# Optimization experiments

Measured on AMD Instinct MI355X. Metric: run time of the kernel, lower is better.

The kernel has to match this reference:

```python
import jax, jax.numpy as jnp
import numpy as np


def _mlp(x, W1, b1, W2, b2, W3, b3):
    # flatten -> fc(784,512) -> relu -> fc(512,128) -> relu -> fc(128,C)
    h = x.reshape(x.shape[0], -1)
    h = jax.nn.relu(h @ W1.T + b1)
    h = jax.nn.relu(h @ W2.T + b2)
    return h @ W3.T + b3


def setup_inputs() -> dict:
    key = jax.random.key(0)
    ks = jax.random.split(key, 6)
    B, Bu, C, D = 65536, 4096, 10, 28 * 28
    return {
        "x": jax.random.uniform(ks[0], (B, 28, 28), jnp.float32),
        "y": jax.random.randint(ks[1], (B,), 0, C),
        "x_unlab": jax.random.uniform(ks[2], (Bu, 28, 28), jnp.float32),
        "W1": jax.random.normal(ks[3], (512, D), jnp.float32) * 0.03,
        "b1": jnp.zeros((512,), jnp.float32),
        "W2": jax.random.normal(ks[4], (128, 512), jnp.float32) * 0.05,
        "b2": jnp.zeros((128,), jnp.float32),
        "W3": jax.random.normal(ks[5], (C, 128), jnp.float32) * 0.08,
        "b3": jnp.zeros((C,), jnp.float32),
    }


def reference(x, y, x_unlab, W1, b1, W2, b2, W3, b3):
    n_classes = W3.shape[0]
    # ---- labeled branch: BCEWithLogitsLoss(mean) vs one-hot targets ----
    logits = _mlp(x, W1, b1, W2, b2, W3, b3)  # [B, C]
    t = jax.nn.one_hot(y, n_classes, dtype=logits.dtype)
    bce = jnp.mean(jnp.maximum(logits, 0.0) - logits * t
                   + jnp.log1p(jnp.exp(-jnp.abs(logits))))
    # ---- unlabeled branch: semantic loss ----
    # sem_loss(probs): s[c] = sum_i p_i[c] * prod_{j != i} (1 - p_j[c]);
    # return mean over classes of -log(s). Done in log domain with a single
    # O(Bu) leave-one-out sum instead of the original O(Bu^2) double loop.
    o_u = _mlp(x_unlab, W1, b1, W2, b2, W3, b3)       # [Bu, C]
    logp = jax.nn.log_sigmoid(o_u)                     # log p
    log1mp = jax.nn.log_sigmoid(-o_u)                  # log (1 - p)
    loo = jnp.sum(log1mp, axis=0, keepdims=True) - log1mp  # leave-one-out log-prod
    log_s = jax.scipy.special.logsumexp(logp + loo, axis=0)  # [C]
    sl = jnp.mean(-log_s)
    # compute_loss returns (bce, sl); stacked here as a length-2 vector
    return jnp.stack([bce, sl])
```

## Files before the change

kernel.cpp:

```cpp
#include <hip/hip_runtime.h>
#include <hip/hip_bf16.h>
#include <stdint.h>

typedef unsigned short ushort_t;
typedef __bf16 bf16x8 __attribute__((ext_vector_type(8)));
typedef float f32x4 __attribute__((ext_vector_type(4)));

__device__ __forceinline__ ushort_t f2bf(float f) {
    union { float f; unsigned u; } v; v.f = f;
    unsigned u = v.u;
    unsigned r = u + 0x7fffu + ((u >> 16) & 1u);
    return (ushort_t)(r >> 16);
}
__device__ __forceinline__ float bf2f(ushort_t h) {
    union { unsigned u; float f; } v; v.u = ((unsigned)h) << 16;
    return v.f;
}

#define GLDS16(gsrc, ldst)                                                    \
    __builtin_amdgcn_global_load_lds(                                         \
        (const __attribute__((address_space(1))) void*)(gsrc),                \
        (__attribute__((address_space(3))) void*)(ldst), 16, 0, 0)

__global__ __launch_bounds__(256) void prep_kernel(
    const float* __restrict__ W1, const float* __restrict__ W2,
    ushort_t* __restrict__ W1p, ushort_t* __restrict__ W2b,
    float* __restrict__ stats)
{
    int idx = blockIdx.x * 256 + threadIdx.x;
    if (idx < 512 * 800) {
        int n = idx / 800, k = idx - n * 800;
        W1p[idx] = (k < 784) ? f2bf(W1[n * 784 + k]) : (ushort_t)0;
    }
    if (idx < 128 * 512) W2b[idx] = f2bf(W2[idx]);
    if (idx == 0) stats[0] = 0.0f;
}

__global__ __launch_bounds__(256) void gemm1_kernel(
    const float* __restrict__ x, const float* __restrict__ xu,
    const ushort_t* __restrict__ W1p, const float* __restrict__ b1,
    ushort_t* __restrict__ h1)
{
    __shared__ ushort_t As[128 * 32];
    __shared__ ushort_t Bs[128 * 32];

    const int tile_n = blockIdx.x & 3;
    const int tile_m = blockIdx.x >> 2;
    const int tid = threadIdx.x;
    const int w = tid >> 6, lane = tid & 63;
    const int wm = w >> 1, wn = w & 1;
    const int quad = lane >> 4, lc = lane & 15;

    const int arow = tid >> 1;
    const int akoff = (tid & 1) * 16;
    const int grow = tile_m * 128 + arow;
    const float* asrc = (grow < 65536) ? (x + (size_t)grow * 784)
                                       : (xu + (size_t)(grow - 65536) * 784);
    const int brow_in = (lane >> 2);
    const int bkoff = (lane & 3) * 8;

    f32x4 acc[4][4];
#pragma unroll
    for (int i = 0; i < 4; i++)
#pragma unroll
        for (int j = 0; j < 4; j++)
#pragma unroll
            for (int r = 0; r < 4; r++) acc[i][j][r] = 0.0f;

    for (int k0 = 0; k0 < 800; k0 += 32) {
#pragma unroll
        for (int c = 0; c < 2; c++) {
            int row = (w * 2 + c) * 16 + brow_in;
            const ushort_t* src =
                W1p + (size_t)(tile_n * 128 + row) * 800 + k0 + bkoff;
            GLDS16(src, Bs + (w * 2 + c) * 512);
        }
        {
            int kch = k0 + akoff;
            uint4 lo, hi;
            if (kch < 784) {
                const float4* p = (const float4*)(asrc + kch);
                float4 f0 = p[0], f1 = p[1], f2 = p[2], f3 = p[3];
                lo.x = ((unsigned)f2bf(f0.y) << 16) | f2bf(f0.x);
                lo.y = ((unsigned)f2bf(f0.w) << 16) | f2bf(f0.z);
                lo.z = ((unsigned)f2bf(f1.y) << 16) | f2bf(f1.x);
                lo.w = ((unsigned)f2bf(f1.w) << 16) | f2bf(f1.z);
                hi.x = ((unsigned)f2bf(f2.y) << 16) | f2bf(f2.x);
                hi.y = ((unsigned)f2bf(f2.w) << 16) | f2bf(f2.z);
                hi.z = ((unsigned)f2bf(f3.y) << 16) | f2bf(f3.x);
                hi.w = ((unsigned)f2bf(f3.w) << 16) | f2bf(f3.z);
            } else {
                lo = make_uint4(0, 0, 0, 0);
                hi = make_uint4(0, 0, 0, 0);
            }
            *(uint4*)&As[arow * 32 + akoff] = lo;
            *(uint4*)&As[arow * 32 + akoff + 8] = hi;
        }
        __syncthreads();

        bf16x8 af[4], bfr[4];
#pragma unroll
        for (int i = 0; i < 4; i++)
            af[i] = *(const bf16x8*)&As[(wm * 64 + i * 16 + lc) * 32 + quad * 8];
#pragma unroll
        for (int j = 0; j < 4; j++)
            bfr[j] = *(const bf16x8*)&Bs[(wn * 64 + j * 16 + lc) * 32 + quad * 8];
#pragma unroll
        for (int i = 0; i < 4; i++)
#pragma unroll
            for (int j = 0; j < 4; j++)
                acc[i][j] = __builtin_amdgcn_mfma_f32_16x16x32_bf16(
                    af[i], bfr[j], acc[i][j], 0, 0, 0);
        __syncthreads();
    }

    float bias[4];
#pragma unroll
    for (int j = 0; j < 4; j++)
        bias[j] = b1[tile_n * 128 + wn * 64 + j * 16 + lc];
#pragma unroll
    for (int i = 0; i < 4; i++) {
        int gr0 = tile_m * 128 + wm * 64 + i * 16 + quad * 4;
#pragma unroll
        for (int j = 0; j < 4; j++) {
            int gc = tile_n * 128 + wn * 64 + j * 16 + lc;
#pragma unroll
            for (int r = 0; r < 4; r++) {
                float v = acc[i][j][r] + bias[j];
                v = fmaxf(v, 0.0f);
                h1[(size_t)(gr0 + r) * 512 + gc] = f2bf(v);
            }
        }
    }
}

__global__ __launch_bounds__(256) void gemm2_kernel(
    const ushort_t* __restrict__ h1, const ushort_t* __restrict__ W2b,
    const float* __restrict__ b2, ushort_t* __restrict__ h2)
{
    __shared__ ushort_t As[128 * 32];
    __shared__ ushort_t Bs[128 * 32];

    const int tile_m = blockIdx.x;
    const int tid = threadIdx.x;
    const int w = tid >> 6, lane = tid & 63;
    const int wm = w >> 1, wn = w & 1;
    const int quad = lane >> 4, lc = lane & 15;
    const int row_in = (lane >> 2);
    const int koff = (lane & 3) * 8;

    f32x4 acc[4][4];
#pragma unroll
    for (int i = 0; i < 4; i++)
#pragma unroll
        for (int j = 0; j < 4; j++)
#pragma unroll
            for (int r = 0; r < 4; r++) acc[i][j][r] = 0.0f;

    for (int k0 = 0; k0 < 512; k0 += 32) {
#pragma unroll
        for (int c = 0; c < 2; c++) {
            int row = (w * 2 + c) * 16 + row_in;
            const ushort_t* srcA =
                h1 + (size_t)(tile_m * 128 + row) * 512 + k0 + koff;
            GLDS16(srcA, As + (w * 2 + c) * 512);
            const ushort_t* srcB = W2b + (size_t)row * 512 + k0 + koff;
            GLDS16(srcB, Bs + (w * 2 + c) * 512);
        }
        __syncthreads();

        bf16x8 af[4], bfr[4];
#pragma unroll
        for (int i = 0; i < 4; i++)
            af[i] = *(const bf16x8*)&As[(wm * 64 + i * 16 + lc) * 32 + quad * 8];
#pragma unroll
        for (int j = 0; j < 4; j++)
            bfr[j] = *(const bf16x8*)&Bs[(wn * 64 + j * 16 + lc) * 32 + quad * 8];
#pragma unroll
        for (int i = 0; i < 4; i++)
#pragma unroll
            for (int j = 0; j < 4; j++)
                acc[i][j] = __builtin_amdgcn_mfma_f32_16x16x32_bf16(
                    af[i], bfr[j], acc[i][j], 0, 0, 0);
        __syncthreads();
    }

    float bias[4];
#pragma unroll
    for (int j = 0; j < 4; j++) bias[j] = b2[wn * 64 + j * 16 + lc];
#pragma unroll
    for (int i = 0; i < 4; i++) {
        int gr0 = tile_m * 128 + wm * 64 + i * 16 + quad * 4;
#pragma unroll
        for (int j = 0; j < 4; j++) {
            int gc = wn * 64 + j * 16 + lc;
#pragma unroll
            for (int r = 0; r < 4; r++) {
                float v = acc[i][j][r] + bias[j];
                v = fmaxf(v, 0.0f);
                h2[(size_t)(gr0 + r) * 128 + gc] = f2bf(v);
            }
        }
    }
}

__global__ __launch_bounds__(256) void loss_kernel(
    const ushort_t* __restrict__ h2, const int* __restrict__ y,
    const float* __restrict__ W3, const float* __restrict__ b3,
    float* __restrict__ stats, float* __restrict__ logits_u)
{
    __shared__ float W3s[10 * 128];
    __shared__ float b3s[10];
    __shared__ ushort_t h2s[64 * 128];
    __shared__ float red[4];

    const int tid = threadIdx.x;
    for (int i = tid; i < 1280; i += 256) W3s[i] = W3[i];
    if (tid < 10) b3s[tid] = b3[tid];

    const size_t row0 = (size_t)blockIdx.x * 64;
    const ushort_t* src = h2 + row0 * 128;
#pragma unroll
    for (int i = tid * 8; i < 64 * 128; i += 256 * 8)
        *(uint4*)&h2s[i] = *(const uint4*)&src[i];
    __syncthreads();

    float bce_part = 0.0f;
    for (int o = tid; o < 640; o += 256) {
        int r = o / 10, c = o - r * 10;
        size_t grow = row0 + r;
        float acc = b3s[c];
        const ushort_t* hr = &h2s[r * 128];
        const float* wr = &W3s[c * 128];
#pragma unroll 8
        for (int k = 0; k < 128; k++) acc += bf2f(hr[k]) * wr[k];
        if (grow < 65536) {
            float t = (y[grow] == c) ? 1.0f : 0.0f;
            bce_part += fmaxf(acc, 0.0f) - acc * t +
                        log1pf(__expf(-fabsf(acc)));
        } else {
            logits_u[(grow - 65536) * 10 + c] = acc;
        }
    }
#pragma unroll
    for (int s = 32; s > 0; s >>= 1) bce_part += __shfl_down(bce_part, s, 64);
    if ((tid & 63) == 0) red[tid >> 6] = bce_part;
    __syncthreads();
    if (tid == 0) {
        float v = red[0] + red[1] + red[2] + red[3];
        atomicAdd(stats, v);
    }
}

__global__ __launch_bounds__(512) void finisher_kernel(
    const float* __restrict__ logits_u, const float* __restrict__ stats,
    float* __restrict__ out)
{
    __shared__ float Rs[32][16];
    __shared__ float Rm[32][16];
    __shared__ float Scol[16], Mcol[16];

    const int tid = threadIdx.x;
    const int c = tid & 15, g = tid >> 4;
    float s = 0.0f, m = -1e30f;
    if (c < 10) {
        for (int i = g; i < 4096; i += 32) {
            float o = logits_u[i * 10 + c];
            s += fminf(-o, 0.0f) - log1pf(__expf(-fabsf(o)));
            m = fmaxf(m, o);
        }
    }
    Rs[g][c] = s;
    Rm[g][c] = m;
    __syncthreads();
    if (tid < 16) {
        float ss = 0.0f, mm = -1e30f;
        for (int gg = 0; gg < 32; gg++) {
            ss += Rs[gg][tid];
            mm = fmaxf(mm, Rm[gg][tid]);
        }
        Scol[tid] = ss;
        Mcol[tid] = mm;
    }
    __syncthreads();
    float e = 0.0f;
    if (c < 10) {
        float mm = Mcol[c];
        for (int i = g; i < 4096; i += 32)
            e += __expf(logits_u[i * 10 + c] - mm);
    }
    Rs[g][c] = e;
    __syncthreads();
    if (tid == 0) {
        float sl = 0.0f;
        for (int cc = 0; cc < 10; cc++) {
            float ee = 0.0f;
            for (int gg = 0; gg < 32; gg++) ee += Rs[gg][cc];
            sl += -(Scol[cc] + Mcol[cc] + __logf(ee));
        }
        sl *= 0.1f;
        out[0] = stats[0] * (1.0f / (65536.0f * 10.0f));
        out[1] = sl;
    }
}

extern "C" void kernel_launch(void* const* d_in, const int* in_sizes, int n_in,
                              void* d_out, int out_size, void* d_ws,
                              size_t ws_size, hipStream_t stream)
{
    const float* x  = (const float*)d_in[0];
    const int*   y  = (const int*)d_in[1];
    const float* xu = (const float*)d_in[2];
    const float* W1 = (const float*)d_in[3];
    const float* b1 = (const float*)d_in[4];
    const float* W2 = (const float*)d_in[5];
    const float* b2 = (const float*)d_in[6];
    const float* W3 = (const float*)d_in[7];
    const float* b3 = (const float*)d_in[8];
    float* out = (float*)d_out;

    char* ws = (char*)d_ws;
    ushort_t* W1p      = (ushort_t*)(ws + 0);
    ushort_t* W2b      = (ushort_t*)(ws + 819200);
    float*    stats    = (float*)(ws + 950272);
    float*    logits_u = (float*)(ws + 950528);
    ushort_t* h1       = (ushort_t*)(ws + 1114368);
    ushort_t* h2       = (ushort_t*)(ws + 72417536);

    prep_kernel<<<1600, 256, 0, stream>>>(W1, W2, W1p, W2b, stats);
    gemm1_kernel<<<544 * 4, 256, 0, stream>>>(x, xu, W1p, b1, h1);
    gemm2_kernel<<<544, 256, 0, stream>>>(h1, W2b, b2, h2);
    loss_kernel<<<1088, 256, 0, stream>>>(h2, y, W3, b3, stats, logits_u);
    finisher_kernel<<<1, 512, 0, stream>>>(logits_u, stats, out);
    (void)in_sizes; (void)n_in; (void)out_size; (void)ws_size;
}
```

Baseline: 572.8 us.

## Pre-convert inputs to bf16 buffer, XCD-aware gemm1 tiling, smaller gemm2 tiles

Adds a separate pass that converts the fp32 inputs into a padded bf16 buffer, so gemm1 can stream A tiles with direct global-to-LDS loads instead of converting fp32 inline on every tile. gemm1 also remaps block indices so consecutive M tiles stay on the same XCD, which should improve L2 reuse of shared A rows. gemm2 moves to 64-row tiles to launch twice as many blocks, and the finisher uses 640 threads with no idle lanes. The cost is an extra full read and write of the input, plus a larger workspace; a fallback path is kept for when the workspace is too small.

```diff
diff --git a/kernel.cpp b/kernel.cpp
--- a/kernel.cpp
+++ b/kernel.cpp
@@ -36,7 +36,112 @@
     if (idx == 0) stats[0] = 0.0f;
 }
 
+__global__ __launch_bounds__(256) void xconvert_kernel(
+    const float* __restrict__ x, const float* __restrict__ xu,
+    ushort_t* __restrict__ Xb)
+{
+    int idx = blockIdx.x * 256 + threadIdx.x;
+    int r = idx / 50, c = idx - r * 50;
+    uint4 lo, hi;
+    if (c < 49) {
+        const float* src = (r < 65536) ? (x + (size_t)r * 784)
+                                       : (xu + (size_t)(r - 65536) * 784);
+        const float4* p = (const float4*)(src + c * 16);
+        float4 f0 = p[0], f1 = p[1], f2 = p[2], f3 = p[3];
+        lo.x = ((unsigned)f2bf(f0.y) << 16) | f2bf(f0.x);
+        lo.y = ((unsigned)f2bf(f0.w) << 16) | f2bf(f0.z);
+        lo.z = ((unsigned)f2bf(f1.y) << 16) | f2bf(f1.x);
+        lo.w = ((unsigned)f2bf(f1.w) << 16) | f2bf(f1.z);
+        hi.x = ((unsigned)f2bf(f2.y) << 16) | f2bf(f2.x);
+        hi.y = ((unsigned)f2bf(f2.w) << 16) | f2bf(f2.z);
+        hi.z = ((unsigned)f2bf(f3.y) << 16) | f2bf(f3.x);
+        hi.w = ((unsigned)f2bf(f3.w) << 16) | f2bf(f3.z);
+    } else {
+        lo = make_uint4(0, 0, 0, 0);
+        hi = make_uint4(0, 0, 0, 0);
+    }
+    uint4* dst = (uint4*)(Xb + (size_t)r * 800 + c * 16);
+    dst[0] = lo;
+    dst[1] = hi;
+}
+
 __global__ __launch_bounds__(256) void gemm1_kernel(
+    const ushort_t* __restrict__ Xb, const ushort_t* __restrict__ W1p,
+    const float* __restrict__ b1, ushort_t* __restrict__ h1)
+{
+    __shared__ ushort_t As[128 * 32];
+    __shared__ ushort_t Bs[128 * 32];
+
+    const int b = blockIdx.x;
+    const int xcd = b & 7, s = b >> 3;
+    const int tile_n = s & 3;
+    const int tile_m = xcd * 68 + (s >> 2);
+
+    const int tid = threadIdx.x;
+    const int w = tid >> 6, lane = tid & 63;
+    const int wm = w >> 1, wn = w & 1;
+    const int quad = lane >> 4, lc = lane & 15;
+    const int row_in = lane >> 2;
+    const int koff = (lane & 3) * 8;
+
+    f32x4 acc[4][4];
+#pragma unroll
+    for (int i = 0; i < 4; i++)
+#pragma unroll
+        for (int j = 0; j < 4; j++)
+#pragma unroll
+            for (int r = 0; r < 4; r++) acc[i][j][r] = 0.0f;
+
+    for (int k0 = 0; k0 < 800; k0 += 32) {
+#pragma unroll
+        for (int c = 0; c < 2; c++) {
+            int row = (w * 2 + c) * 16 + row_in;
+            const ushort_t* srcA =
+                Xb + (size_t)(tile_m * 128 + row) * 800 + k0 + koff;
+            GLDS16(srcA, As + (w * 2 + c) * 512);
+            const ushort_t* srcB =
+                W1p + (size_t)(tile_n * 128 + row) * 800 + k0 + koff;
+            GLDS16(srcB, Bs + (w * 2 + c) * 512);
+        }
+        __syncthreads();
+
+        bf16x8 af[4], bfr[4];
+#pragma unroll
+        for (int i = 0; i < 4; i++)
+            af[i] = *(const bf16x8*)&As[(wm * 64 + i * 16 + lc) * 32 + quad * 8];
+#pragma unroll
+        for (int j = 0; j < 4; j++)
+            bfr[j] = *(const bf16x8*)&Bs[(wn * 64 + j * 16 + lc) * 32 + quad * 8];
+#pragma unroll
+        for (int i = 0; i < 4; i++)
+#pragma unroll
+            for (int j = 0; j < 4; j++)
+                acc[i][j] = __builtin_amdgcn_mfma_f32_16x16x32_bf16(
+                    af[i], bfr[j], acc[i][j], 0, 0, 0);
+        __syncthreads();
+    }
+
+    float bias[4];
+#pragma unroll
+    for (int j = 0; j < 4; j++)
+        bias[j] = b1[tile_n * 128 + wn * 64 + j * 16 + lc];
+#pragma unroll
+    for (int i = 0; i < 4; i++) {
+        int gr0 = tile_m * 128 + wm * 64 + i * 16 + quad * 4;
+#pragma unroll
+        for (int j = 0; j < 4; j++) {
+            int gc = tile_n * 128 + wn * 64 + j * 16 + lc;
+#pragma unroll
+            for (int r = 0; r < 4; r++) {
+                float v = acc[i][j][r] + bias[j];
+                v = fmaxf(v, 0.0f);
+                h1[(size_t)(gr0 + r) * 512 + gc] = f2bf(v);
+            }
+        }
+    }
+}
+
+__global__ __launch_bounds__(256) void gemm1_inline_kernel(
     const float* __restrict__ x, const float* __restrict__ xu,
     const ushort_t* __restrict__ W1p, const float* __restrict__ b1,
     ushort_t* __restrict__ h1)
@@ -138,7 +243,7 @@
     const ushort_t* __restrict__ h1, const ushort_t* __restrict__ W2b,
     const float* __restrict__ b2, ushort_t* __restrict__ h2)
 {
-    __shared__ ushort_t As[128 * 32];
+    __shared__ ushort_t As[64 * 32];
     __shared__ ushort_t Bs[128 * 32];
 
     const int tile_m = blockIdx.x;
@@ -146,38 +251,41 @@
     const int w = tid >> 6, lane = tid & 63;
     const int wm = w >> 1, wn = w & 1;
     const int quad = lane >> 4, lc = lane & 15;
-    const int row_in = (lane >> 2);
+    const int row_in = lane >> 2;
     const int koff = (lane & 3) * 8;
 
-    f32x4 acc[4][4];
-#pragma unroll
-    for (int i = 0; i < 4; i++)
+    f32x4 acc[2][4];
+#pragma unroll
+    for (int i = 0; i < 2; i++)
 #pragma unroll
         for (int j = 0; j < 4; j++)
 #pragma unroll
             for (int r = 0; r < 4; r++) acc[i][j][r] = 0.0f;
 
     for (int k0 = 0; k0 < 512; k0 += 32) {
+        {
+            int row = w * 16 + row_in;
+            const ushort_t* srcA =
+                h1 + (size_t)(tile_m * 64 + row) * 512 + k0 + koff;
+            GLDS16(srcA, As + w * 512);
+        }
 #pragma unroll
         for (int c = 0; c < 2; c++) {
             int row = (w * 2 + c) * 16 + row_in;
-            const ushort_t* srcA =
-                h1 + (size_t)(tile_m * 128 + row) * 512 + k0 + koff;
-            GLDS16(srcA, As + (w * 2 + c) * 512);
             const ushort_t* srcB = W2b + (size_t)row * 512 + k0 + koff;
             GLDS16(srcB, Bs + (w * 2 + c) * 512);
         }
         __syncthreads();
 
-        bf16x8 af[4], bfr[4];
-#pragma unroll
-        for (int i = 0; i < 4; i++)
-            af[i] = *(const bf16x8*)&As[(wm * 64 + i * 16 + lc) * 32 + quad * 8];
+        bf16x8 af[2], bfr[4];
+#pragma unroll
+        for (int i = 0; i < 2; i++)
+            af[i] = *(const bf16x8*)&As[(wm * 32 + i * 16 + lc) * 32 + quad * 8];
 #pragma unroll
         for (int j = 0; j < 4; j++)
             bfr[j] = *(const bf16x8*)&Bs[(wn * 64 + j * 16 + lc) * 32 + quad * 8];
 #pragma unroll
-        for (int i = 0; i < 4; i++)
+        for (int i = 0; i < 2; i++)
 #pragma unroll
             for (int j = 0; j < 4; j++)
                 acc[i][j] = __builtin_amdgcn_mfma_f32_16x16x32_bf16(
@@ -189,8 +297,8 @@
 #pragma unroll
     for (int j = 0; j < 4; j++) bias[j] = b2[wn * 64 + j * 16 + lc];
 #pragma unroll
-    for (int i = 0; i < 4; i++) {
-        int gr0 = tile_m * 128 + wm * 64 + i * 16 + quad * 4;
+    for (int i = 0; i < 2; i++) {
+        int gr0 = tile_m * 64 + wm * 32 + i * 16 + quad * 4;
 #pragma unroll
         for (int j = 0; j < 4; j++) {
             int gc = wn * 64 + j * 16 + lc;
@@ -252,30 +360,28 @@
     }
 }
 
-__global__ __launch_bounds__(512) void finisher_kernel(
+__global__ __launch_bounds__(640) void finisher_kernel(
     const float* __restrict__ logits_u, const float* __restrict__ stats,
     float* __restrict__ out)
 {
-    __shared__ float Rs[32][16];
-    __shared__ float Rm[32][16];
-    __shared__ float Scol[16], Mcol[16];
+    __shared__ float Rs[64][10];
+    __shared__ float Rm[64][10];
+    __shared__ float Scol[10], Mcol[10];
 
     const int tid = threadIdx.x;
-    const int c = tid & 15, g = tid >> 4;
+    const int g = tid / 10, c = tid - g * 10;
     float s = 0.0f, m = -1e30f;
-    if (c < 10) {
-        for (int i = g; i < 4096; i += 32) {
-            float o = logits_u[i * 10 + c];
-            s += fminf(-o, 0.0f) - log1pf(__expf(-fabsf(o)));
-            m = fmaxf(m, o);
-        }
+    for (int i = g; i < 4096; i += 64) {
+        float o = logits_u[i * 10 + c];
+        s += fminf(-o, 0.0f) - log1pf(__expf(-fabsf(o)));
+        m = fmaxf(m, o);
     }
     Rs[g][c] = s;
     Rm[g][c] = m;
     __syncthreads();
-    if (tid < 16) {
+    if (tid < 10) {
         float ss = 0.0f, mm = -1e30f;
-        for (int gg = 0; gg < 32; gg++) {
+        for (int gg = 0; gg < 64; gg++) {
             ss += Rs[gg][tid];
             mm = fmaxf(mm, Rm[gg][tid]);
         }
@@ -284,18 +390,16 @@
     }
     __syncthreads();
     float e = 0.0f;
-    if (c < 10) {
-        float mm = Mcol[c];
-        for (int i = g; i < 4096; i += 32)
-            e += __expf(logits_u[i * 10 + c] - mm);
-    }
+    float mm = Mcol[c];
+    for (int i = g; i < 4096; i += 64)
+        e += __expf(logits_u[i * 10 + c] - mm);
     Rs[g][c] = e;
     __syncthreads();
     if (tid == 0) {
         float sl = 0.0f;
         for (int cc = 0; cc < 10; cc++) {
             float ee = 0.0f;
-            for (int gg = 0; gg < 32; gg++) ee += Rs[gg][cc];
+            for (int gg = 0; gg < 64; gg++) ee += Rs[gg][cc];
             sl += -(Scol[cc] + Mcol[cc] + __logf(ee));
         }
         sl *= 0.1f;
@@ -326,11 +430,18 @@
     float*    logits_u = (float*)(ws + 950528);
     ushort_t* h1       = (ushort_t*)(ws + 1114368);
     ushort_t* h2       = (ushort_t*)(ws + 72417536);
+    ushort_t* Xb       = (ushort_t*)(ws + 72417536);
+    const size_t FAST_WS_NEED = 183828736;
 
     prep_kernel<<<1600, 256, 0, stream>>>(W1, W2, W1p, W2b, stats);
-    gemm1_kernel<<<544 * 4, 256, 0, stream>>>(x, xu, W1p, b1, h1);
-    gemm2_kernel<<<544, 256, 0, stream>>>(h1, W2b, b2, h2);
+    if (ws_size >= FAST_WS_NEED) {
+        xconvert_kernel<<<13600, 256, 0, stream>>>(x, xu, Xb);
+        gemm1_kernel<<<2176, 256, 0, stream>>>(Xb, W1p, b1, h1);
+    } else {
+        gemm1_inline_kernel<<<2176, 256, 0, stream>>>(x, xu, W1p, b1, h1);
+    }
+    gemm2_kernel<<<1088, 256, 0, stream>>>(h1, W2b, b2, h2);
     loss_kernel<<<1088, 256, 0, stream>>>(h2, y, W3, b3, stats, logits_u);
-    finisher_kernel<<<1, 512, 0, stream>>>(logits_u, stats, out);
+    finisher_kernel<<<1, 640, 0, stream>>>(logits_u, stats, out);
     (void)in_sizes; (void)n_in; (void)out_size; (void)ws_size;
 }
```

After: 552.9 us. -3.5%, faster.
